# Kernel tuning notes

Measured on AMD Instinct MI355X. Metric: run time of the kernel, lower is better.

## Reference

```python
import jax, jax.numpy as jnp
import numpy as np

B, C, S, E, H = 16, 24, 128, 256, 8
P = E // H  # head projection dim (consistent interpretation of the buggy source)
EPS = 1e-6


def _ln(x, g, b):
    mu = jnp.mean(x, axis=-1, keepdims=True)
    var = jnp.mean((x - mu) ** 2, axis=-1, keepdims=True)
    return (x - mu) * jax.lax.rsqrt(var + EPS) * g + b


def setup_inputs() -> dict:
    key = jax.random.key(0)
    ks = jax.random.split(key, 16)
    s = 0.02
    return {
        'x': jax.random.normal(ks[0], (B, C, S, E), jnp.float32),
        # spatial attention params
        'Wq_s': s * jax.random.normal(ks[1], (H, C, P, E), jnp.float32),
        'Wk_s': s * jax.random.normal(ks[2], (H, E, P), jnp.float32),
        'Wv_s': s * jax.random.normal(ks[3], (H, E, P), jnp.float32),
        'Wo_s': s * jax.random.normal(ks[4], (C, E, E), jnp.float32),
        # temporal attention params
        'Wq_t': s * jax.random.normal(ks[5], (H, C, E, P), jnp.float32),
        'Wk_t': s * jax.random.normal(ks[6], (H, C, E, P), jnp.float32),
        'Wv_t': s * jax.random.normal(ks[7], (H, C, E, P), jnp.float32),
        'Wo_t': s * jax.random.normal(ks[8], (C, E, E), jnp.float32),
        # shared layernorm
        'ln_g': jnp.ones((E,), jnp.float32),
        'ln_b': jnp.zeros((E,), jnp.float32),
        # per-joint pointwise FF (Linear->ReLU->Linear)
        'ff_w1': s * jax.random.normal(ks[9], (C, E, E), jnp.float32),
        'ff_b1': jnp.zeros((C, E), jnp.float32),
        'ff_w2': s * jax.random.normal(ks[10], (C, E, E), jnp.float32),
        'ff_b2': jnp.zeros((C, E), jnp.float32),
    }


def _spatial_attention(x, Wq, Wk, Wv, Wo):
    # x: [B,C,S,E]; per-head per-joint query proj, shared key/value proj
    q = jnp.einsum('bcse,hcpe->bshcp', x, Wq)          # [B,S,H,C,P]
    k = jnp.einsum('bcse,hep->bshcp', x, Wk)
    v = jnp.einsum('bcse,hep->bshcp', x, Wv)
    scores = jnp.einsum('bshcp,bshdp->bshcd', q, k) / jnp.sqrt(jnp.float32(P))
    a = jax.nn.softmax(scores, axis=-1)                # attn over joints d
    o = jnp.einsum('bshcd,bshdp->bshcp', a, v)
    o = o.transpose(0, 3, 1, 2, 4).reshape(x.shape[0], C, x.shape[2], H * P)  # [B,C,S,E]
    return jnp.einsum('bcse,cef->bcsf', o, Wo)


def _temporal_attention(x, Wq, Wk, Wv, Wo):
    q = jnp.einsum('bcse,hcep->bhcsp', x, Wq)          # [B,H,C,S,P]
    k = jnp.einsum('bcse,hcep->bhcsp', x, Wk)
    v = jnp.einsum('bcse,hcep->bhcsp', x, Wv)
    scores = jnp.einsum('bhcsp,bhctp->bhcst', q, k) / jnp.sqrt(jnp.float32(P))
    a = jax.nn.softmax(scores, axis=-1)                # attn over time t
    o = jnp.einsum('bhcst,bhctp->bhcsp', a, v)
    o = o.transpose(0, 2, 3, 1, 4).reshape(x.shape[0], C, x.shape[2], H * P)  # [B,C,S,E]
    return jnp.einsum('bcse,cef->bcsf', o, Wo)


def reference(x, Wq_s, Wk_s, Wv_s, Wo_s, Wq_t, Wk_t, Wv_t, Wo_t, ln_g, ln_b, ff_w1, ff_b1, ff_w2, ff_b2):
    spat = _spatial_attention(x, Wq_s, Wk_s, Wv_s, Wo_s)
    temp = _temporal_attention(x, Wq_t, Wk_t, Wv_t, Wo_t)
    attn_out = _ln(x + spat, ln_g, ln_b) + _ln(x + temp, ln_g, ln_b)
    # per-joint pointwise FF, vectorized over joints
    h = jax.nn.relu(jnp.einsum('bcse,cef->bcsf', attn_out, ff_w1) + ff_b1[None, :, None, :])
    ff = jnp.einsum('bcse,cef->bcsf', h, ff_w2) + ff_b2[None, :, None, :]
    return _ln(attn_out + ff, ln_g, ln_b)
```

## Files before the change

### kernel.cpp

```cpp
#include <hip/hip_runtime.h>
#include <hip/hip_bf16.h>

constexpr int Bn = 16, Cn = 24, Sn = 128, En = 256, Hn = 8, Pn = 32;
constexpr size_t NBUF = (size_t)Bn * Cn * Sn * En;
constexpr size_t WSLOT = (size_t)Cn * 256 * 256;

typedef __bf16 bf16_t;
typedef bf16_t bf16x8 __attribute__((ext_vector_type(8)));
typedef bf16_t bf16x4 __attribute__((ext_vector_type(4)));
typedef float f32x4 __attribute__((ext_vector_type(4)));

__device__ __forceinline__ void gl2lds16(const bf16_t* g, bf16_t* l) {
    typedef const __attribute__((address_space(1))) unsigned int* gp_t;
    typedef __attribute__((address_space(3))) unsigned int* lp_t;
    __builtin_amdgcn_global_load_lds((gp_t)(unsigned long long)g,
                                     (lp_t)(unsigned int)(unsigned long long)l,
                                     16, 0, 0);
}

__global__ __launch_bounds__(256) void conv_x_k(const float* __restrict__ x,
                                                bf16_t* __restrict__ xb) {
    const size_t i = ((size_t)blockIdx.x * 256 + threadIdx.x) * 4;
    const float4 v = *(const float4*)(x + i);
    bf16x4 o = {(bf16_t)v.x, (bf16_t)v.y, (bf16_t)v.z, (bf16_t)v.w};
// ... 1 lines not shown
}

__global__ __launch_bounds__(256) void conv_w_copy_k(const float* __restrict__ W,
                                                     bf16_t* __restrict__ out) {
    const int row = blockIdx.x * 4 + (threadIdx.x >> 6);
    const int lane = threadIdx.x & 63;
    const int n = row & 255, c = row >> 8;
    const float* src = W + (size_t)c * (Pn * En) + (size_t)(n >> 5) * (Cn * Pn * En) +
                       (size_t)(n & 31) * En + lane * 4;
    const float4 v = *(const float4*)src;
    bf16x4 o = {(bf16_t)v.x, (bf16_t)v.y, (bf16_t)v.z, (bf16_t)v.w};
    *(bf16x4*)(out + (size_t)row * 256 + lane * 4) = o;
}

struct TDesc { const float* W; int Sc, Snh, Se; };

__global__ __launch_bounds__(256) void conv_w_tr_k(
    TDesc d0, TDesc d1, TDesc d2, TDesc d3, TDesc d4,
    bf16_t* __restrict__ out)
{
    TDesc d;
    switch (blockIdx.z) {
        case 0: d = d0; break; case 1: d = d1; break; case 2: d = d2; break;
        case 3: d = d3; break; default: d = d4; break;
    }
    const int g = blockIdx.x & 7, et = blockIdx.x >> 3;
    const int c = blockIdx.y;

    __shared__ float tile[32][65];

    const int t = threadIdx.x;
    const float* base = d.W + (size_t)c * d.Sc + (size_t)g * d.Snh;

#pragma unroll
    for (int pass = 0; pass < 2; ++pass) {
        const int e_local = pass * 32 + (t >> 3);
        const int j4 = (t & 7) * 4;
        const float4 v = *(const float4*)(base + (size_t)(et * 64 + e_local) * d.Se + j4);
        tile[j4 + 0][e_local] = v.x;
        tile[j4 + 1][e_local] = v.y;
        tile[j4 + 2][e_local] = v.z;
        tile[j4 + 3][e_local] = v.w;
    }
    __syncthreads();

    const int j = t >> 3, e8 = (t & 7) * 8;
    bf16x8 o;
#pragma unroll
    for (int k = 0; k < 8; ++k) o[k] = (bf16_t)tile[j][e8 + k];
    *(bf16x8*)(out + (size_t)blockIdx.z * WSLOT +
               ((size_t)c * 256 + g * 32 + j) * 256 + et * 64 + e8) = o;
}

__global__ __launch_bounds__(256) void conv_w_k(const float* __restrict__ W,
                                                bf16_t* __restrict__ Wb,
                                                int Sc, int Snh, int Snp, int Se) {
    const int n = blockIdx.x & 255, c = blockIdx.x >> 8;
    const int e = threadIdx.x;
    Wb[(size_t)blockIdx.x * 256 + e] =
        (bf16_t)W[(size_t)c * Sc + (size_t)(n >> 5) * Snh + (n & 31) * Snp + (size_t)e * Se];
}

struct GDesc { const bf16_t* W; bf16_t* O; int Aoff, Wc, Ob, Oc, Os, Onh, Onp, trans; };

template <int NP>
__global__ __launch_bounds__(256) void gemm_mfma(
    const bf16_t* __restrict__ A, int Ab, int Ac, int As,
    GDesc g0, GDesc g1, GDesc g2)
{
    const int b = blockIdx.x, c = blockIdx.z;
    const int proj = (NP == 1) ? 0 : ((int)blockIdx.y >> 1);
    const int nt = (NP == 1) ? (int)blockIdx.y : ((int)blockIdx.y & 1);
    GDesc g = (proj == 0) ? g0 : (proj == 1) ? g1 : g2;

    __shared__ bf16_t smem[3][2][128 * 32];
    bf16_t* Cs = &smem[0][0][0];

    const int tid = threadIdx.x, wv = tid >> 6, ln = tid & 63;
    const int wm = (wv >> 1) * 64, wn = (wv & 1) * 64;
    const int lr = ln & 15, hi = ln >> 4;

    const bf16_t* Abase = A + g.Aoff + (size_t)b * Ab + (size_t)c * Ac;
    const bf16_t* Bbase = g.W + (size_t)c * g.Wc + (size_t)(nt * 128) * 256;

    auto stage = [&](int buf, int kt) {
        const int k0 = kt * 32;
#pragma unroll
        for (int it = 0; it < 2; ++it) {
            const int cb = it * 256 + wv * 64;
            const int mc = cb + ln;
            const int row = mc >> 2;
            const int kc = (((mc & 3) ^ ((row >> 1) & 3)) * 8);
            gl2lds16(Abase + (size_t)row * As + k0 + kc, &smem[buf][0][cb * 8]);
            gl2lds16(Bbase + (size_t)row * 256 + k0 + kc, &smem[buf][1][cb * 8]);
        }
    };

    f32x4 acc[4][4] = {};

    stage(0, 0);
    stage(1, 1);

#pragma unroll
    for (int kt = 0; kt < 8; ++kt) {
        if (kt < 6) stage((kt + 2) % 3, kt + 2);
        if (kt < 6)       asm volatile("s_waitcnt vmcnt(8)" ::: "memory");
        else if (kt == 6) asm volatile("s_waitcnt vmcnt(4)" ::: "memory");
        else              asm volatile("s_waitcnt vmcnt(0)" ::: "memory");
        __builtin_amdgcn_s_barrier();
        __builtin_amdgcn_sched_barrier(0);

        const int cur = kt % 3;
        bf16x8 af[4], bfr[4];
// ... 26 lines not shown
#pragma unroll
                for (int i = 0; i < 4; ++i)
#pragma unroll
                    for (int j = 0; j < 4; ++j)
#pragma unroll
                        for (int r = 0; r < 4; ++r)
                            Cs[(i * 16 + hi * 4 + r) * 136 + wn + j * 16 + lr] =
                                (bf16_t)acc[i][j][r];
            }
            __syncthreads();
#pragma unroll
            for (int it = 0; it < 2; ++it) {
                const int lrow = it * 32 + (tid >> 3);
                const int n0 = (tid & 7) * 16;
                bf16x8 v0 = *(const bf16x8*)&Cs[lrow * 136 + n0];
                bf16x8 v1 = *(const bf16x8*)&Cs[lrow * 136 + n0 + 8];
                const int m = pass * 64 + lrow;
                const int n = nt * 128 + n0;
                bf16_t* dst = g.O + (size_t)b * g.Ob + (size_t)c * g.Oc +
                              (size_t)m * g.Os + (size_t)(n >> 5) * g.Onh + (n & 31);
                *(bf16x8*)dst = v0;
                *(bf16x8*)(dst + 8) = v1;
            }
            __syncthreads();
        } else {
            if (wn == pass * 64) {
#pragma unroll
                for (int i = 0; i < 4; ++i)
#pragma unroll
                    for (int j = 0; j < 4; ++j) {
                        bf16x4 pk = {(bf16_t)acc[i][j][0], (bf16_t)acc[i][j][1],
                                     (bf16_t)acc[i][j][2], (bf16_t)acc[i][j][3]};
                        *(bf16x4*)&Cs[(j * 16 + lr) * 136 + wm + i * 16 + hi * 4] = pk;
                    }
            }
            __syncthreads();
#pragma unroll
            for (int it = 0; it < 2; ++it) {
                const int lrow = it * 32 + (tid >> 3);
                const int m0 = (tid & 7) * 16;
                bf16x8 v0 = *(const bf16x8*)&Cs[lrow * 136 + m0];
                bf16x8 v1 = *(const bf16x8*)&Cs[lrow * 136 + m0 + 8];
                const int n = nt * 128 + pass * 64 + lrow;
                bf16_t* dst = g.O + (size_t)b * g.Ob + (size_t)c * g.Oc +
                              (size_t)(n >> 5) * g.Onh + (size_t)(n & 31) * g.Onp + m0;
                *(bf16x8*)dst = v0;
                *(bf16x8*)(dst + 8) = v1;
            }
            __syncthreads();
        }
    }
}

__global__ __launch_bounds__(256) void wo_ln_fused(
    const bf16_t* __restrict__ A1, const bf16_t* __restrict__ A2,
    const bf16_t* __restrict__ W1, const bf16_t* __restrict__ W2,
    const bf16_t* __restrict__ xb, const float* __restrict__ g,
    const float* __restrict__ beta, bf16_t* __restrict__ AO)
{
    const int bx = blockIdx.x, c = blockIdx.z;
    const int R = ((bx >> 1) * Cn + c) * Sn + (bx & 1) * 64;

    __shared__ bf16_t lds[33792];

    const int tid = threadIdx.x, wv = tid >> 6, ln = tid & 63;
    const int wn = wv * 64, lr = ln & 15, hi = ln >> 4;

    const bf16_t* Ab0 = A1 + (size_t)R * 256;
    const bf16_t* Ab1 = A2 + (size_t)R * 256;
    const bf16_t* Wb0 = W1 + (size_t)c * 65536;
    const bf16_t* Wb1 = W2 + (size_t)c * 65536;

    auto stage = [&](int buf, int t) {
        const bf16_t* Asrc = (t < 8) ? Ab0 : Ab1;
        const bf16_t* Wsrc = (t < 8) ? Wb0 : Wb1;
        const int k0 = (t & 7) * 32;
        bf16_t* base = &lds[buf * 10240];
        {
            const int ch = wv * 64 + ln;
            const int row = ch >> 2;
            const int kc = (((ch & 3) ^ ((row >> 1) & 3)) * 8);
            gl2lds16(Asrc + (size_t)row * 256 + k0 + kc, base + ch * 8);
        }
#pragma unroll
        for (int g2 = 0; g2 < 4; ++g2) {
            const int ch = g2 * 256 + wv * 64 + ln;
            const int row = ch >> 2;
            const int kc = (((ch & 3) ^ ((row >> 1) & 3)) * 8);
            gl2lds16(Wsrc + (size_t)row * 256 + k0 + kc, base + 2048 + ch * 8);
        }
    };

    f32x4 accS[4][4] = {}, accT[4][4] = {};

    stage(0, 0);
#pragma unroll
    for (int t = 0; t < 16; ++t) {
        if (t < 15) {
            stage((t + 1) & 1, t + 1);
            asm volatile("s_waitcnt vmcnt(5)" ::: "memory");
        } else {
            asm volatile("s_waitcnt vmcnt(0)" ::: "memory");
        }
        __builtin_amdgcn_s_barrier();
        __builtin_amdgcn_sched_barrier(0);

        const bf16_t* base = &lds[(t & 1) * 10240];
        bf16x8 af[4], bfr[4];
#pragma unroll
        for (int i = 0; i < 4; ++i) {
            const int r = i * 16 + lr;
            af[i] = *(const bf16x8*)(base + r * 32 + ((hi ^ ((r >> 1) & 3)) * 8));
        }
#pragma unroll
        for (int j = 0; j < 4; ++j) {
            const int r = wn + j * 16 + lr;
            bfr[j] = *(const bf16x8*)(base + 2048 + r * 32 + ((hi ^ ((r >> 1) & 3)) * 8));
        }
        __builtin_amdgcn_s_setprio(1);
        if (t < 8) {
#pragma unroll
            for (int i = 0; i < 4; ++i)
#pragma unroll
                for (int j = 0; j < 4; ++j)
                    accS[i][j] = __builtin_amdgcn_mfma_f32_16x16x32_bf16(af[i], bfr[j], accS[i][j], 0, 0, 0);
        } else {
#pragma unroll
            for (int i = 0; i < 4; ++i)
#pragma unroll
                for (int j = 0; j < 4; ++j)
                    accT[i][j] = __builtin_amdgcn_mfma_f32_16x16x32_bf16(af[i], bfr[j], accT[i][j], 0, 0, 0);
        }
        __builtin_amdgcn_s_setprio(0);
        __builtin_amdgcn_sched_barrier(0);
        __builtin_amdgcn_s_barrier();
    }

    bf16_t* Ss = &lds[0];
    bf16_t* Ts = &lds[16896];
#pragma unroll
    for (int i = 0; i < 4; ++i)
#pragma unroll
        for (int j = 0; j < 4; ++j)
#pragma unroll
            for (int r = 0; r < 4; ++r) {
                const int m = i * 16 + hi * 4 + r;
                const int n = wn + j * 16 + lr;
                Ss[m * 264 + n] = (bf16_t)accS[i][j][r];
                Ts[m * 264 + n] = (bf16_t)accT[i][j][r];
            }
    __syncthreads();

    const int row = tid >> 2, c0 = (tid & 3) * 64;
    const bf16_t* xp = xb + (size_t)(R + row) * 256 + c0;
    bf16x8 xv[8];
    float s1 = 0, q1 = 0, s2 = 0, q2 = 0;
#pragma unroll
    for (int u = 0; u < 8; ++u) {
        xv[u] = *(const bf16x8*)(xp + u * 8);
        bf16x8 sv = *(const bf16x8*)&Ss[row * 264 + c0 + u * 8];
        bf16x8 tv = *(const bf16x8*)&Ts[row * 264 + c0 + u * 8];
#pragma unroll
        for (int e = 0; e < 8; ++e) {
            const float xf = (float)xv[u][e];
            const float a = xf + (float)sv[e];
            const float t2 = xf + (float)tv[e];
            s1 += a; q1 += a * a; s2 += t2; q2 += t2 * t2;
        }
    }
    s1 += __shfl_xor(s1, 1); s1 += __shfl_xor(s1, 2);
    q1 += __shfl_xor(q1, 1); q1 += __shfl_xor(q1, 2);
    s2 += __shfl_xor(s2, 1); s2 += __shfl_xor(s2, 2);
    q2 += __shfl_xor(q2, 1); q2 += __shfl_xor(q2, 2);
    const float mu1 = s1 / 256.f, mu2 = s2 / 256.f;
    const float r1 = rsqrtf(q1 / 256.f - mu1 * mu1 + 1e-6f);
    const float r2 = rsqrtf(q2 / 256.f - mu2 * mu2 + 1e-6f);
#pragma unroll
    for (int u = 0; u < 8; ++u) {
        bf16x8 sv = *(const bf16x8*)&Ss[row * 264 + c0 + u * 8];
        bf16x8 tv = *(const bf16x8*)&Ts[row * 264 + c0 + u * 8];
        bf16x8 o8;
#pragma unroll
        for (int e = 0; e < 8; ++e) {
            const int n = c0 + u * 8 + e;
            const float xf = (float)xv[u][e];
            const float a = xf + (float)sv[e];
            const float t2 = xf + (float)tv[e];
            o8[e] = (bf16_t)((a - mu1) * r1 * g[n] + (t2 - mu2) * r2 * g[n] + 2.f * beta[n]);
        }
        *(bf16x8*)(AO + (size_t)(R + row) * 256 + c0 + u * 8) = o8;
    }
}

__global__ __launch_bounds__(256) void ff_ln_fused(
    const bf16_t* __restrict__ AO, const bf16_t* __restrict__ W1,
    const bf16_t* __restrict__ W2, const float* __restrict__ b1v,
    const float* __restrict__ b2v, const float* __restrict__ g,
    const float* __restrict__ beta, float* __restrict__ out)
{
    const int bx = blockIdx.x, c = blockIdx.z;
    const int R = ((bx >> 1) * Cn + c) * Sn + (bx & 1) * 64;

    __shared__ bf16_t lds[37376];

    const int tid = threadIdx.x, wv = tid >> 6, ln = tid & 63;
    const int wn = wv * 64, lr = ln & 15, hi = ln >> 4;

    const bf16_t* Abase = AO + (size_t)R * 256;
    const bf16_t* W1b = W1 + (size_t)c * 65536;
    const bf16_t* W2b = W2 + (size_t)c * 65536;
    bf16_t* Hs = &lds[20480];

    auto stageA = [&](int buf, int kt) {
        const int k0 = kt * 32;
        const int ch = wv * 64 + ln;
        const int row = ch >> 2;
        const int kc = (((ch & 3) ^ ((row >> 1) & 3)) * 8);
        gl2lds16(Abase + (size_t)row * 256 + k0 + kc, &lds[buf * 10240] + ch * 8);
    };
    auto stageB = [&](int buf, int kt, const bf16_t* Wsrc) {
        const int k0 = kt * 32;
#pragma unroll
        for (int g2 = 0; g2 < 4; ++g2) {
            const int ch = g2 * 256 + wv * 64 + ln;
            const int row = ch >> 2;
            const int kc = (((ch & 3) ^ ((row >> 1) & 3)) * 8);
            gl2lds16(Wsrc + (size_t)row * 256 + k0 + kc, &lds[buf * 10240] + 2048 + ch * 8);
        }
    };

    f32x4 acc[4][4] = {};

    stageA(0, 0); stageB(0, 0, W1b);
#pragma unroll
    for (int t = 0; t < 8; ++t) {
        if (t < 7) {
            stageA((t + 1) & 1, t + 1); stageB((t + 1) & 1, t + 1, W1b);
            asm volatile("s_waitcnt vmcnt(5)" ::: "memory");
        } else {
            asm volatile("s_waitcnt vmcnt(0)" ::: "memory");
        }
        __builtin_amdgcn_s_barrier();
        __builtin_amdgcn_sched_barrier(0);
        const bf16_t* base = &lds[(t & 1) * 10240];
        bf16x8 af[4], bfr[4];
#pragma unroll
        for (int i = 0; i < 4; ++i) {
            const int r = i * 16 + lr;
            af[i] = *(const bf16x8*)(base + r * 32 + ((hi ^ ((r >> 1) & 3)) * 8));
        }
#pragma unroll
        for (int j = 0; j < 4; ++j) {
            const int r = wn + j * 16 + lr;
            bfr[j] = *(const bf16x8*)(base + 2048 + r * 32 + ((hi ^ ((r >> 1) & 3)) * 8));
        }
        __builtin_amdgcn_s_setprio(1);
#pragma unroll
        for (int i = 0; i < 4; ++i)
#pragma unroll
            for (int j = 0; j < 4; ++j)
                acc[i][j] = __builtin_amdgcn_mfma_f32_16x16x32_bf16(af[i], bfr[j], acc[i][j], 0, 0, 0);
        __builtin_amdgcn_s_setprio(0);
        __builtin_amdgcn_sched_barrier(0);
        __builtin_amdgcn_s_barrier();
    }

    stageB(0, 0, W2b);
#pragma unroll
    for (int i = 0; i < 4; ++i)
#pragma unroll
        for (int j = 0; j < 4; ++j) {
            const int n = wn + j * 16 + lr;
            const float bv = b1v[c * 256 + n];
#pragma unroll
            for (int r = 0; r < 4; ++r)
                Hs[(i * 16 + hi * 4 + r) * 264 + n] =
                    (bf16_t)fmaxf(acc[i][j][r] + bv, 0.f);
        }
    __syncthreads();

    f32x4 acc2[4][4] = {};
#pragma unroll
    for (int t = 0; t < 8; ++t) {
        if (t < 7) {
            stageB((t + 1) & 1, t + 1, W2b);
            asm volatile("s_waitcnt vmcnt(4)" ::: "memory");
        } else {
            asm volatile("s_waitcnt vmcnt(0)" ::: "memory");
        }
        __builtin_amdgcn_s_barrier();
        __builtin_amdgcn_sched_barrier(0);
        const bf16_t* base = &lds[(t & 1) * 10240];
        bf16x8 af[4], bfr[4];
#pragma unroll
        for (int i = 0; i < 4; ++i)
            af[i] = *(const bf16x8*)&Hs[(i * 16 + lr) * 264 + t * 32 + hi * 8];
#pragma unroll
        for (int j = 0; j < 4; ++j) {
            const int r = wn + j * 16 + lr;
            bfr[j] = *(const bf16x8*)(base + 2048 + r * 32 + ((hi ^ ((r >> 1) & 3)) * 8));
        }
        __builtin_amdgcn_s_setprio(1);
#pragma unroll
        for (int i = 0; i < 4; ++i)
#pragma unroll
            for (int j = 0; j < 4; ++j)
                acc2[i][j] = __builtin_amdgcn_mfma_f32_16x16x32_bf16(af[i], bfr[j], acc2[i][j], 0, 0, 0);
        __builtin_amdgcn_s_setprio(0);
        __builtin_amdgcn_sched_barrier(0);
        __builtin_amdgcn_s_barrier();
    }

    bf16_t* Fs = &lds[0];
#pragma unroll
    for (int i = 0; i < 4; ++i)
#pragma unroll
        for (int j = 0; j < 4; ++j) {
            const int n = wn + j * 16 + lr;
            const float bv = b2v[c * 256 + n];
#pragma unroll
            for (int r = 0; r < 4; ++r)
                Fs[(i * 16 + hi * 4 + r) * 264 + n] = (bf16_t)(acc2[i][j][r] + bv);
        }
    __syncthreads();

    const int row = tid >> 2, c0 = (tid & 3) * 64;
    const bf16_t* ap = AO + (size_t)(R + row) * 256 + c0;
    bf16x8 av[8];
    float s = 0, q = 0;
#pragma unroll
    for (int u = 0; u < 8; ++u) {
        av[u] = *(const bf16x8*)(ap + u * 8);
        bf16x8 fv = *(const bf16x8*)&Fs[row * 264 + c0 + u * 8];
#pragma unroll
        for (int e = 0; e < 8; ++e) {
            const float a = (float)av[u][e] + (float)fv[e];
            s += a; q += a * a;
        }
    }
    s += __shfl_xor(s, 1); s += __shfl_xor(s, 2);
    q += __shfl_xor(q, 1); q += __shfl_xor(q, 2);
    const float mu = s / 256.f;
    const float rin = rsqrtf(q / 256.f - mu * mu + 1e-6f);
#pragma unroll
    for (int u = 0; u < 8; ++u) {
        bf16x8 fv = *(const bf16x8*)&Fs[row * 264 + c0 + u * 8];
        float4 o0, o1;
        float* op = &o0.x;
#pragma unroll
        for (int e = 0; e < 8; ++e) {
            const int n = c0 + u * 8 + e;
            const float a = (float)av[u][e] + (float)fv[e];
            const float v = (a - mu) * rin * g[n] + beta[n];
            if (e < 4) (&o0.x)[e] = v; else (&o1.x)[e - 4] = v;
        }
        (void)op;
        float* dst = out + (size_t)(R + row) * 256 + c0 + u * 8;
        *(float4*)dst = o0;
        *(float4*)(dst + 4) = o1;
    }
}

__global__ __launch_bounds__(256) void attn_spatial_mfma(
    const bf16_t* __restrict__ Q, const bf16_t* __restrict__ K,
    const bf16_t* __restrict__ V, bf16_t* __restrict__ O)
{
    __shared__ bf16_t Ps[4][32 * 40];
    __shared__ bf16_t Vt[4][32 * 40];

    const int tid = threadIdx.x, wv = tid >> 6, ln = tid & 63;
    const int lr = ln & 15, hi = ln >> 4, lk = hi * 8;

    const int bsh = blockIdx.x * 4 + wv;
    const int h = bsh & 7, s = (bsh >> 3) & 127, b = bsh >> 10;
    const size_t qb = (size_t)bsh * (Cn * Pn);

    {
        const int p = ln >> 1, c0 = 24 + (ln & 1) * 4;
        bf16x4 z = {};
        *(bf16x4*)&Vt[wv][p * 40 + c0] = z;
    }
#pragma unroll
    for (int it = 0; it < 2; ++it) {
        const int ch = it * 64 + ln;
        if (ch < 96) {
            const int cc = ch >> 2, p0 = (ch & 3) * 8;
            bf16x8 v = *(const bf16x8*)(V + qb + cc * 32 + p0);
#pragma unroll
            for (int j = 0; j < 8; ++j)
                Vt[wv][(p0 + j) * 40 + cc] = v[j];
        }
    }

    bf16x8 aq0 = *(const bf16x8*)(Q + qb + lr * 32 + lk);
    bf16x8 aq1 = *(const bf16x8*)(Q + qb + (16 + lr) * 32 + lk);
    bf16x8 bk0 = *(const bf16x8*)(K + qb + lr * 32 + lk);
    bf16x8 bk1 = *(const bf16x8*)(K + qb + (16 + lr) * 32 + lk);
    const f32x4 zz = {0.f, 0.f, 0.f, 0.f};
    f32x4 sc[2][2];
    sc[0][0] = __builtin_amdgcn_mfma_f32_16x16x32_bf16(aq0, bk0, zz, 0, 0, 0);
    sc[0][1] = __builtin_amdgcn_mfma_f32_16x16x32_bf16(aq0, bk1, zz, 0, 0, 0);
    sc[1][0] = __builtin_amdgcn_mfma_f32_16x16x32_bf16(aq1, bk0, zz, 0, 0, 0);
    sc[1][1] = __builtin_amdgcn_mfma_f32_16x16x32_bf16(aq1, bk1, zz, 0, 0, 0);

    const float scale = 0.17677669529663687f;
#pragma unroll
    for (int i = 0; i < 2; ++i) {
        float s0[4], s1[4], mx[4];
#pragma unroll
        for (int r = 0; r < 4; ++r) {
            s0[r] = sc[i][0][r] * scale;
            s1[r] = (lr >= 8) ? -3.0e38f : sc[i][1][r] * scale;
// ... 139 lines not shown
        bf16x8 bv0 = *(const bf16x8*)&Vs[lr * 136 + kk * 32 + lk];
        bf16x8 bv1 = *(const bf16x8*)&Vs[(16 + lr) * 136 + kk * 32 + lk];
        o[0][0] = __builtin_amdgcn_mfma_f32_16x16x32_bf16(ap0, bv0, o[0][0], 0, 0, 0);
        o[0][1] = __builtin_amdgcn_mfma_f32_16x16x32_bf16(ap0, bv1, o[0][1], 0, 0, 0);
        o[1][0] = __builtin_amdgcn_mfma_f32_16x16x32_bf16(ap1, bv0, o[1][0], 0, 0, 0);
        o[1][1] = __builtin_amdgcn_mfma_f32_16x16x32_bf16(ap1, bv1, o[1][1], 0, 0, 0);
    }

#pragma unroll
    for (int i = 0; i < 2; ++i) {
        const int sb = r0 + i * 16 + (ln >> 4) * 4;
#pragma unroll
        for (int j = 0; j < 2; ++j) {
            const int p = h * 32 + j * 16 + lr;
#pragma unroll
            for (int r = 0; r < 4; ++r)
                O[((size_t)(b * Cn + c) * Sn + (sb + r)) * En + p] = (bf16_t)o[i][j][r];
        }
    }
}

extern "C" void kernel_launch(void* const* d_in, const int* in_sizes, int n_in,
                              void* d_out, int out_size, void* d_ws, size_t ws_size,
                              hipStream_t stream)
{
    const float* x     = (const float*)d_in[0];
    const float* Wq_s  = (const float*)d_in[1];
    const float* Wk_s  = (const float*)d_in[2];
    const float* Wv_s  = (const float*)d_in[3];
    const float* Wo_s  = (const float*)d_in[4];
    const float* Wq_t  = (const float*)d_in[5];
    const float* Wk_t  = (const float*)d_in[6];
    const float* Wv_t  = (const float*)d_in[7];
    const float* Wo_t  = (const float*)d_in[8];
    const float* ln_g  = (const float*)d_in[9];
    const float* ln_b  = (const float*)d_in[10];
    const float* ff_w1 = (const float*)d_in[11];
    const float* ff_b1 = (const float*)d_in[12];
    const float* ff_w2 = (const float*)d_in[13];
    const float* ff_b2 = (const float*)d_in[14];
    float* out = (float*)d_out;

    bf16_t* wsb = (bf16_t*)d_ws;
    bf16_t* b0 = wsb;
    bf16_t* b1 = wsb + NBUF;
    bf16_t* b2 = wsb + 2 * NBUF;
    bf16_t* b3 = wsb + 3 * NBUF;
    bf16_t* b4 = wsb + 4 * NBUF;

    bf16_t* xb = (bf16_t*)d_out;
    bf16_t* wb = xb + NBUF;
    bf16_t* w_qs = wb + 0 * WSLOT;
    bf16_t* wtr  = wb + 1 * WSLOT;
    bf16_t* w_os = wtr + 0 * WSLOT;
    bf16_t* w_qt = wtr + 1 * WSLOT;
    bf16_t* w_kt = wtr + 2 * WSLOT;
    bf16_t* w_vt = wtr + 3 * WSLOT;
    bf16_t* w_ot = wtr + 4 * WSLOT;
    bf16_t* w_ks = b4 + NBUF - 2 * 65536;
    bf16_t* w_vs = b4 + NBUF - 65536;
    bf16_t* w_f1 = b0;
    bf16_t* w_f2 = b0 + WSLOT;

    const int XAb = Cn * Sn * En, XAc = Sn * En, XAs = En;
    const int QSb = Sn * Hn * Cn * Pn, QSs = Hn * Cn * Pn, QSh = Cn * Pn;
    const int QTb = Hn * Cn * Sn * Pn, QTh = Cn * Sn * Pn, QTc = Sn * Pn, QTs = Pn;
    const int WCP = 256 * 256;

    conv_x_k<<<NBUF / 1024, 256, 0, stream>>>(x, xb);
    conv_w_copy_k<<<1536, 256, 0, stream>>>(Wq_s, w_qs);
    conv_w_tr_k<<<dim3(32, 24, 5), 256, 0, stream>>>(
        TDesc{Wo_s, En * En, Pn, En},
        TDesc{Wq_t, En * Pn, Cn * En * Pn, Pn},
        TDesc{Wk_t, En * Pn, Cn * En * Pn, Pn},
        TDesc{Wv_t, En * Pn, Cn * En * Pn, Pn},
        TDesc{Wo_t, En * En, Pn, En},
        wtr);
    conv_w_k<<<256, 256, 0, stream>>>(Wk_s, w_ks, 0, En * Pn, 1, Pn);
    conv_w_k<<<256, 256, 0, stream>>>(Wv_s, w_vs, 0, En * Pn, 1, Pn);

    gemm_mfma<3><<<dim3(16, 6, 24), 256, 0, stream>>>(
        xb, XAb, XAc, XAs,
        GDesc{w_qs, b0, 0, WCP, QSb, Pn, QSs, QSh, 1, 0},
        GDesc{w_ks, b1, 0, 0,   QSb, Pn, QSs, QSh, 1, 0},
        GDesc{w_vs, b2, 0, 0,   QSb, Pn, QSs, QSh, 1, 0});
    attn_spatial_mfma<<<Bn * Sn * Hn / 4, 256, 0, stream>>>(b0, b1, b2, b3);

    gemm_mfma<3><<<dim3(16, 6, 24), 256, 0, stream>>>(
        xb, XAb, XAc, XAs,
        GDesc{w_qt, b0, 0, WCP, QTb, QTc, QTs, QTh, 1, 0},
        GDesc{w_kt, b1, 0, WCP, QTb, QTc, QTs, QTh, 1, 0},
        GDesc{w_vt, b2, 0, WCP, QTb, QTc, 1, QTh, Sn, 1});
    attn_temporal_mfma<<<dim3(24, 8, 16), 256, 0, stream>>>(b0, b1, b2, b4);

    conv_w_tr_k<<<dim3(32, 24, 2), 256, 0, stream>>>(
        TDesc{ff_w1, En * En, Pn, En},
        TDesc{ff_w2, En * En, Pn, En},
        TDesc{ff_w1, En * En, Pn, En},
        TDesc{ff_w1, En * En, Pn, En},
        TDesc{ff_w1, En * En, Pn, En},
        w_f1);

    wo_ln_fused<<<dim3(32, 1, 24), 256, 0, stream>>>(
        b3, b4, w_os, w_ot, xb, ln_g, ln_b, b2);

    ff_ln_fused<<<dim3(32, 1, 24), 256, 0, stream>>>(
        b2, w_f1, w_f2, ff_b1, ff_b2, ln_g, ln_b, out);
}
```

Measured before the change: 387.3 us.

## Fuse output projections, layernorms and feed-forward into one epilogue kernel

Merges the Wo/LayerNorm kernel and the FF/LayerNorm kernel into a single epilogue kernel. The attention-sum activation now stays in registers and LDS instead of going to global memory as bf16 and being read back. The two Wo GEMMs run in sequence with a shared accumulator to lower register pressure. The residual x is read directly as fp32 rather than from the bf16 copy. Weight conversion launches are also regrouped: the Wk_s/Wv_s conversions become one launch, and the Wo transposes move to the later conversion launch. In exchange the kernel is longer and has more barriers.

```diff
diff --git a/kernel.cpp b/kernel.cpp
--- a/kernel.cpp
+++ b/kernel.cpp
@@ -77,13 +77,15 @@
                ((size_t)c * 256 + g * 32 + j) * 256 + et * 64 + e8) = o;
 }
 
-__global__ __launch_bounds__(256) void conv_w_k(const float* __restrict__ W,
-                                                bf16_t* __restrict__ Wb,
-                                                int Sc, int Snh, int Snp, int Se) {
-    const int n = blockIdx.x & 255, c = blockIdx.x >> 8;
-    const int e = threadIdx.x;
-    Wb[(size_t)blockIdx.x * 256 + e] =
-        (bf16_t)W[(size_t)c * Sc + (size_t)(n >> 5) * Snh + (n & 31) * Snp + (size_t)e * Se];
+__global__ __launch_bounds__(256) void conv_w_k2(const float* __restrict__ Wk,
+                                                 const float* __restrict__ Wv,
+                                                 bf16_t* __restrict__ Ok,
+                                                 bf16_t* __restrict__ Ov) {
+    const float* W = blockIdx.y ? Wv : Wk;
+    bf16_t* o = blockIdx.y ? Ov : Ok;
+    const int n = blockIdx.x, e = threadIdx.x;
+    o[(size_t)n * 256 + e] =
+        (bf16_t)W[(size_t)(n >> 5) * (En * Pn) + (n & 31) + (size_t)e * Pn];
 }
 
 struct GDesc { const bf16_t* W; bf16_t* O; int Aoff, Wc, Ob, Oc, Os, Onh, Onp, trans; };
@@ -216,149 +218,11 @@
     }
 }
 
-__global__ __launch_bounds__(256) void wo_ln_fused(
+__global__ __launch_bounds__(256) void epilogue_fused(
     const bf16_t* __restrict__ A1, const bf16_t* __restrict__ A2,
-    const bf16_t* __restrict__ W1, const bf16_t* __restrict__ W2,
-    const bf16_t* __restrict__ xb, const float* __restrict__ g,
-    const float* __restrict__ beta, bf16_t* __restrict__ AO)
-{
-    const int bx = blockIdx.x, c = blockIdx.z;
-    const int R = ((bx >> 1) * Cn + c) * Sn + (bx & 1) * 64;
-
-    __shared__ bf16_t lds[33792];
-
-    const int tid = threadIdx.x, wv = tid >> 6, ln = tid & 63;
-    const int wn = wv * 64, lr = ln & 15, hi = ln >> 4;
-
-    const bf16_t* Ab0 = A1 + (size_t)R * 256;
-    const bf16_t* Ab1 = A2 + (size_t)R * 256;
-    const bf16_t* Wb0 = W1 + (size_t)c * 65536;
-    const bf16_t* Wb1 = W2 + (size_t)c * 65536;
-
-    auto stage = [&](int buf, int t) {
-        const bf16_t* Asrc = (t < 8) ? Ab0 : Ab1;
-        const bf16_t* Wsrc = (t < 8) ? Wb0 : Wb1;
-        const int k0 = (t & 7) * 32;
-        bf16_t* base = &lds[buf * 10240];
-        {
-            const int ch = wv * 64 + ln;
-            const int row = ch >> 2;
-            const int kc = (((ch & 3) ^ ((row >> 1) & 3)) * 8);
-            gl2lds16(Asrc + (size_t)row * 256 + k0 + kc, base + ch * 8);
-        }
-#pragma unroll
-        for (int g2 = 0; g2 < 4; ++g2) {
-            const int ch = g2 * 256 + wv * 64 + ln;
-            const int row = ch >> 2;
-            const int kc = (((ch & 3) ^ ((row >> 1) & 3)) * 8);
-            gl2lds16(Wsrc + (size_t)row * 256 + k0 + kc, base + 2048 + ch * 8);
-        }
-    };
-
-    f32x4 accS[4][4] = {}, accT[4][4] = {};
-
-    stage(0, 0);
-#pragma unroll
-    for (int t = 0; t < 16; ++t) {
-        if (t < 15) {
-            stage((t + 1) & 1, t + 1);
-            asm volatile("s_waitcnt vmcnt(5)" ::: "memory");
-        } else {
-            asm volatile("s_waitcnt vmcnt(0)" ::: "memory");
-        }
-        __builtin_amdgcn_s_barrier();
-        __builtin_amdgcn_sched_barrier(0);
-
-        const bf16_t* base = &lds[(t & 1) * 10240];
-        bf16x8 af[4], bfr[4];
-#pragma unroll
-        for (int i = 0; i < 4; ++i) {
-            const int r = i * 16 + lr;
-            af[i] = *(const bf16x8*)(base + r * 32 + ((hi ^ ((r >> 1) & 3)) * 8));
-        }
-#pragma unroll
-        for (int j = 0; j < 4; ++j) {
-            const int r = wn + j * 16 + lr;
-            bfr[j] = *(const bf16x8*)(base + 2048 + r * 32 + ((hi ^ ((r >> 1) & 3)) * 8));
-        }
-        __builtin_amdgcn_s_setprio(1);
-        if (t < 8) {
-#pragma unroll
-            for (int i = 0; i < 4; ++i)
-#pragma unroll
-                for (int j = 0; j < 4; ++j)
-                    accS[i][j] = __builtin_amdgcn_mfma_f32_16x16x32_bf16(af[i], bfr[j], accS[i][j], 0, 0, 0);
-        } else {
-#pragma unroll
-            for (int i = 0; i < 4; ++i)
-#pragma unroll
-                for (int j = 0; j < 4; ++j)
-                    accT[i][j] = __builtin_amdgcn_mfma_f32_16x16x32_bf16(af[i], bfr[j], accT[i][j], 0, 0, 0);
-        }
-        __builtin_amdgcn_s_setprio(0);
-        __builtin_amdgcn_sched_barrier(0);
-        __builtin_amdgcn_s_barrier();
-    }
-
-    bf16_t* Ss = &lds[0];
-    bf16_t* Ts = &lds[16896];
-#pragma unroll
-    for (int i = 0; i < 4; ++i)
-#pragma unroll
-        for (int j = 0; j < 4; ++j)
-#pragma unroll
-            for (int r = 0; r < 4; ++r) {
-                const int m = i * 16 + hi * 4 + r;
-                const int n = wn + j * 16 + lr;
-                Ss[m * 264 + n] = (bf16_t)accS[i][j][r];
-                Ts[m * 264 + n] = (bf16_t)accT[i][j][r];
-            }
-    __syncthreads();
-
-    const int row = tid >> 2, c0 = (tid & 3) * 64;
-    const bf16_t* xp = xb + (size_t)(R + row) * 256 + c0;
-    bf16x8 xv[8];
-    float s1 = 0, q1 = 0, s2 = 0, q2 = 0;
-#pragma unroll
-    for (int u = 0; u < 8; ++u) {
-        xv[u] = *(const bf16x8*)(xp + u * 8);
-        bf16x8 sv = *(const bf16x8*)&Ss[row * 264 + c0 + u * 8];
-        bf16x8 tv = *(const bf16x8*)&Ts[row * 264 + c0 + u * 8];
-#pragma unroll
-        for (int e = 0; e < 8; ++e) {
-            const float xf = (float)xv[u][e];
-            const float a = xf + (float)sv[e];
-            const float t2 = xf + (float)tv[e];
-            s1 += a; q1 += a * a; s2 += t2; q2 += t2 * t2;
-        }
-    }
-    s1 += __shfl_xor(s1, 1); s1 += __shfl_xor(s1, 2);
-    q1 += __shfl_xor(q1, 1); q1 += __shfl_xor(q1, 2);
-    s2 += __shfl_xor(s2, 1); s2 += __shfl_xor(s2, 2);
-    q2 += __shfl_xor(q2, 1); q2 += __shfl_xor(q2, 2);
-    const float mu1 = s1 / 256.f, mu2 = s2 / 256.f;
-    const float r1 = rsqrtf(q1 / 256.f - mu1 * mu1 + 1e-6f);
-    const float r2 = rsqrtf(q2 / 256.f - mu2 * mu2 + 1e-6f);
-#pragma unroll
-    for (int u = 0; u < 8; ++u) {
-        bf16x8 sv = *(const bf16x8*)&Ss[row * 264 + c0 + u * 8];
-        bf16x8 tv = *(const bf16x8*)&Ts[row * 264 + c0 + u * 8];
-        bf16x8 o8;
-#pragma unroll
-        for (int e = 0; e < 8; ++e) {
-            const int n = c0 + u * 8 + e;
-            const float xf = (float)xv[u][e];
-            const float a = xf + (float)sv[e];
-            const float t2 = xf + (float)tv[e];
-            o8[e] = (bf16_t)((a - mu1) * r1 * g[n] + (t2 - mu2) * r2 * g[n] + 2.f * beta[n]);
-        }
-        *(bf16x8*)(AO + (size_t)(R + row) * 256 + c0 + u * 8) = o8;
-    }
-}
-
-__global__ __launch_bounds__(256) void ff_ln_fused(
-    const bf16_t* __restrict__ AO, const bf16_t* __restrict__ W1,
-    const bf16_t* __restrict__ W2, const float* __restrict__ b1v,
+    const bf16_t* __restrict__ Wos, const bf16_t* __restrict__ Wot,
+    const bf16_t* __restrict__ Wf1, const bf16_t* __restrict__ Wf2,
+    const float* __restrict__ xf, const float* __restrict__ b1v,
     const float* __restrict__ b2v, const float* __restrict__ g,
     const float* __restrict__ beta, float* __restrict__ out)
 {
@@ -369,67 +233,244 @@
 
     const int tid = threadIdx.x, wv = tid >> 6, ln = tid & 63;
     const int wn = wv * 64, lr = ln & 15, hi = ln >> 4;
-
-    const bf16_t* Abase = AO + (size_t)R * 256;
-    const bf16_t* W1b = W1 + (size_t)c * 65536;
-    const bf16_t* W2b = W2 + (size_t)c * 65536;
-    bf16_t* Hs = &lds[20480];
-
-    auto stageA = [&](int buf, int kt) {
+    const int row = tid >> 2, c0 = (tid & 3) * 64;
+
+    const bf16_t* WosB = Wos + (size_t)c * 65536;
+    const bf16_t* WotB = Wot + (size_t)c * 65536;
+    const bf16_t* W1b  = Wf1 + (size_t)c * 65536;
+    const bf16_t* W2b  = Wf2 + (size_t)c * 65536;
+
+    auto stageAW = [&](int buf, int kt, const bf16_t* Asrc, const bf16_t* Wsrc) {
         const int k0 = kt * 32;
-        const int ch = wv * 64 + ln;
-        const int row = ch >> 2;
-        const int kc = (((ch & 3) ^ ((row >> 1) & 3)) * 8);
-        gl2lds16(Abase + (size_t)row * 256 + k0 + kc, &lds[buf * 10240] + ch * 8);
-    };
-    auto stageB = [&](int buf, int kt, const bf16_t* Wsrc) {
-        const int k0 = kt * 32;
+        bf16_t* base = &lds[buf * 10240];
+        {
+            const int ch = wv * 64 + ln;
+            const int r2 = ch >> 2;
+            const int kc = (((ch & 3) ^ ((r2 >> 1) & 3)) * 8);
+            gl2lds16(Asrc + (size_t)r2 * 256 + k0 + kc, base + ch * 8);
+        }
 #pragma unroll
         for (int g2 = 0; g2 < 4; ++g2) {
             const int ch = g2 * 256 + wv * 64 + ln;
-            const int row = ch >> 2;
-            const int kc = (((ch & 3) ^ ((row >> 1) & 3)) * 8);
-            gl2lds16(Wsrc + (size_t)row * 256 + k0 + kc, &lds[buf * 10240] + 2048 + ch * 8);
+            const int r2 = ch >> 2;
+            const int kc = (((ch & 3) ^ ((r2 >> 1) & 3)) * 8);
+            gl2lds16(Wsrc + (size_t)r2 * 256 + k0 + kc, base + 2048 + ch * 8);
         }
     };
-
-    f32x4 acc[4][4] = {};
-
-    stageA(0, 0); stageB(0, 0, W1b);
-#pragma unroll
-    for (int t = 0; t < 8; ++t) {
-        if (t < 7) {
-            stageA((t + 1) & 1, t + 1); stageB((t + 1) & 1, t + 1, W1b);
-            asm volatile("s_waitcnt vmcnt(5)" ::: "memory");
-        } else {
-            asm volatile("s_waitcnt vmcnt(0)" ::: "memory");
-        }
-        __builtin_amdgcn_s_barrier();
-        __builtin_amdgcn_sched_barrier(0);
-        const bf16_t* base = &lds[(t & 1) * 10240];
-        bf16x8 af[4], bfr[4];
-#pragma unroll
-        for (int i = 0; i < 4; ++i) {
-            const int r = i * 16 + lr;
-            af[i] = *(const bf16x8*)(base + r * 32 + ((hi ^ ((r >> 1) & 3)) * 8));
-        }
-#pragma unroll
-        for (int j = 0; j < 4; ++j) {
-            const int r = wn + j * 16 + lr;
-            bfr[j] = *(const bf16x8*)(base + 2048 + r * 32 + ((hi ^ ((r >> 1) & 3)) * 8));
-        }
-        __builtin_amdgcn_s_setprio(1);
+    auto stageW = [&](int buf, int kt, const bf16_t* Wsrc) {
+        const int k0 = kt * 32;
+#pragma unroll
+        for (int g2 = 0; g2 < 4; ++g2) {
+            const int ch = g2 * 256 + wv * 64 + ln;
+            const int r2 = ch >> 2;
+            const int kc = (((ch & 3) ^ ((r2 >> 1) & 3)) * 8);
+            gl2lds16(Wsrc + (size_t)r2 * 256 + k0 + kc,
+                     &lds[20480 + buf * 8192] + ch * 8);
+        }
+    };
+
+    f32x4 acc[4][4];
+    bf16x8 ao_r[8], xv_r[8];
+    bf16_t* STs = &lds[20480];
+
+    {
+        const bf16_t* Ab = A1 + (size_t)R * 256;
 #pragma unroll
         for (int i = 0; i < 4; ++i)
 #pragma unroll
-            for (int j = 0; j < 4; ++j)
-                acc[i][j] = __builtin_amdgcn_mfma_f32_16x16x32_bf16(af[i], bfr[j], acc[i][j], 0, 0, 0);
-        __builtin_amdgcn_s_setprio(0);
-        __builtin_amdgcn_sched_barrier(0);
-        __builtin_amdgcn_s_barrier();
-    }
-
-    stageB(0, 0, W2b);
+            for (int j = 0; j < 4; ++j) acc[i][j] = (f32x4){0.f, 0.f, 0.f, 0.f};
+        stageAW(0, 0, Ab, WosB);
+#pragma unroll
+        for (int t = 0; t < 8; ++t) {
+            if (t < 7) {
+                stageAW((t + 1) & 1, t + 1, Ab, WosB);
+                asm volatile("s_waitcnt vmcnt(5)" ::: "memory");
+            } else asm volatile("s_waitcnt vmcnt(0)" ::: "memory");
+            __builtin_amdgcn_s_barrier();
+            __builtin_amdgcn_sched_barrier(0);
+            const bf16_t* base = &lds[(t & 1) * 10240];
+            bf16x8 af[4], bfr[4];
+#pragma unroll
+            for (int i = 0; i < 4; ++i) {
+                const int r = i * 16 + lr;
+                af[i] = *(const bf16x8*)(base + r * 32 + ((hi ^ ((r >> 1) & 3)) * 8));
+            }
+#pragma unroll
+            for (int j = 0; j < 4; ++j) {
+                const int r = wn + j * 16 + lr;
+                bfr[j] = *(const bf16x8*)(base + 2048 + r * 32 + ((hi ^ ((r >> 1) & 3)) * 8));
+            }
+            __builtin_amdgcn_s_setprio(1);
+#pragma unroll
+            for (int i = 0; i < 4; ++i)
+#pragma unroll
+                for (int j = 0; j < 4; ++j)
+                    acc[i][j] = __builtin_amdgcn_mfma_f32_16x16x32_bf16(af[i], bfr[j], acc[i][j], 0, 0, 0);
+            __builtin_amdgcn_s_setprio(0);
+            __builtin_amdgcn_sched_barrier(0);
+            __builtin_amdgcn_s_barrier();
+        }
+    }
+#pragma unroll
+    for (int i = 0; i < 4; ++i)
+#pragma unroll
+        for (int j = 0; j < 4; ++j)
+#pragma unroll
+            for (int r = 0; r < 4; ++r)
+                STs[(i * 16 + hi * 4 + r) * 264 + wn + j * 16 + lr] = (bf16_t)acc[i][j][r];
+    __syncthreads();
+
+    const bf16_t* Ab2 = A2 + (size_t)R * 256;
+    stageAW(0, 0, Ab2, WotB);
+
+    {
+        const float* xp = xf + (size_t)(R + row) * 256 + c0;
+        float s1 = 0, q1 = 0;
+#pragma unroll
+        for (int u = 0; u < 8; ++u) {
+            const float4 xa = *(const float4*)(xp + u * 8);
+            const float4 xb4 = *(const float4*)(xp + u * 8 + 4);
+            bf16x8 xv;
+            xv[0] = (bf16_t)xa.x; xv[1] = (bf16_t)xa.y; xv[2] = (bf16_t)xa.z; xv[3] = (bf16_t)xa.w;
+            xv[4] = (bf16_t)xb4.x; xv[5] = (bf16_t)xb4.y; xv[6] = (bf16_t)xb4.z; xv[7] = (bf16_t)xb4.w;
+            xv_r[u] = xv;
+            bf16x8 sv = *(const bf16x8*)&STs[row * 264 + c0 + u * 8];
+#pragma unroll
+            for (int e = 0; e < 8; ++e) {
+                const float a = (float)xv[e] + (float)sv[e];
+                s1 += a; q1 += a * a;
+            }
+        }
+        s1 += __shfl_xor(s1, 1); s1 += __shfl_xor(s1, 2);
+        q1 += __shfl_xor(q1, 1); q1 += __shfl_xor(q1, 2);
+        const float mu1 = s1 / 256.f;
+        const float r1 = rsqrtf(q1 / 256.f - mu1 * mu1 + 1e-6f);
+#pragma unroll
+        for (int u = 0; u < 8; ++u) {
+            bf16x8 sv = *(const bf16x8*)&STs[row * 264 + c0 + u * 8];
+            bf16x8 o8;
+#pragma unroll
+            for (int e = 0; e < 8; ++e) {
+                const int n = c0 + u * 8 + e;
+                const float a = (float)xv_r[u][e] + (float)sv[e];
+                o8[e] = (bf16_t)((a - mu1) * r1 * g[n] + beta[n]);
+            }
+            ao_r[u] = o8;
+        }
+    }
+
+    {
+#pragma unroll
+        for (int i = 0; i < 4; ++i)
+#pragma unroll
+            for (int j = 0; j < 4; ++j) acc[i][j] = (f32x4){0.f, 0.f, 0.f, 0.f};
+#pragma unroll
+        for (int t = 0; t < 8; ++t) {
+            if (t < 7) {
+                stageAW((t + 1) & 1, t + 1, Ab2, WotB);
+                asm volatile("s_waitcnt vmcnt(5)" ::: "memory");
+            } else asm volatile("s_waitcnt vmcnt(0)" ::: "memory");
+            __builtin_amdgcn_s_barrier();
+            __builtin_amdgcn_sched_barrier(0);
+            const bf16_t* base = &lds[(t & 1) * 10240];
+            bf16x8 af[4], bfr[4];
+#pragma unroll
+            for (int i = 0; i < 4; ++i) {
+                const int r = i * 16 + lr;
+                af[i] = *(const bf16x8*)(base + r * 32 + ((hi ^ ((r >> 1) & 3)) * 8));
+            }
+#pragma unroll
+            for (int j = 0; j < 4; ++j) {
+                const int r = wn + j * 16 + lr;
+                bfr[j] = *(const bf16x8*)(base + 2048 + r * 32 + ((hi ^ ((r >> 1) & 3)) * 8));
+            }
+            __builtin_amdgcn_s_setprio(1);
+#pragma unroll
+            for (int i = 0; i < 4; ++i)
+#pragma unroll
+                for (int j = 0; j < 4; ++j)
+                    acc[i][j] = __builtin_amdgcn_mfma_f32_16x16x32_bf16(af[i], bfr[j], acc[i][j], 0, 0, 0);
+            __builtin_amdgcn_s_setprio(0);
+            __builtin_amdgcn_sched_barrier(0);
+            __builtin_amdgcn_s_barrier();
+        }
+    }
+#pragma unroll
+    for (int i = 0; i < 4; ++i)
+#pragma unroll
+        for (int j = 0; j < 4; ++j)
+#pragma unroll
+            for (int r = 0; r < 4; ++r)
+                STs[(i * 16 + hi * 4 + r) * 264 + wn + j * 16 + lr] = (bf16_t)acc[i][j][r];
+    __syncthreads();
+
+    {
+        float s2 = 0, q2 = 0;
+#pragma unroll
+        for (int u = 0; u < 8; ++u) {
+            bf16x8 tv = *(const bf16x8*)&STs[row * 264 + c0 + u * 8];
+#pragma unroll
+            for (int e = 0; e < 8; ++e) {
+                const float a = (float)xv_r[u][e] + (float)tv[e];
+                s2 += a; q2 += a * a;
+            }
+        }
+        s2 += __shfl_xor(s2, 1); s2 += __shfl_xor(s2, 2);
+        q2 += __shfl_xor(q2, 1); q2 += __shfl_xor(q2, 2);
+        const float mu2 = s2 / 256.f;
+        const float r2 = rsqrtf(q2 / 256.f - mu2 * mu2 + 1e-6f);
+#pragma unroll
+        for (int u = 0; u < 8; ++u) {
+            bf16x8 tv = *(const bf16x8*)&STs[row * 264 + c0 + u * 8];
+            bf16x8 o8;
+#pragma unroll
+            for (int e = 0; e < 8; ++e) {
+                const int n = c0 + u * 8 + e;
+                const float a = (float)xv_r[u][e] + (float)tv[e];
+                o8[e] = (bf16_t)((float)ao_r[u][e] + (a - mu2) * r2 * g[n] + beta[n]);
+            }
+            ao_r[u] = o8;
+            *(bf16x8*)&lds[row * 264 + c0 + u * 8] = o8;
+        }
+    }
+    __syncthreads();
+
+    {
+#pragma unroll
+        for (int i = 0; i < 4; ++i)
+#pragma unroll
+            for (int j = 0; j < 4; ++j) acc[i][j] = (f32x4){0.f, 0.f, 0.f, 0.f};
+        stageW(0, 0, W1b);
+#pragma unroll
+        for (int t = 0; t < 8; ++t) {
+            if (t < 7) {
+                stageW((t + 1) & 1, t + 1, W1b);
+                asm volatile("s_waitcnt vmcnt(4)" ::: "memory");
+            } else asm volatile("s_waitcnt vmcnt(0)" ::: "memory");
+            __builtin_amdgcn_s_barrier();
+            __builtin_amdgcn_sched_barrier(0);
+            bf16x8 af[4], bfr[4];
+#pragma unroll
+            for (int i = 0; i < 4; ++i)
+                af[i] = *(const bf16x8*)&lds[(i * 16 + lr) * 264 + t * 32 + hi * 8];
+#pragma unroll
+            for (int j = 0; j < 4; ++j) {
+                const int r = wn + j * 16 + lr;
+                bfr[j] = *(const bf16x8*)(&lds[20480 + (t & 1) * 8192] + r * 32 +
+                                          ((hi ^ ((r >> 1) & 3)) * 8));
+            }
+            __builtin_amdgcn_s_setprio(1);
+#pragma unroll
+            for (int i = 0; i < 4; ++i)
+#pragma unroll
+                for (int j = 0; j < 4; ++j)
+                    acc[i][j] = __builtin_amdgcn_mfma_f32_16x16x32_bf16(af[i], bfr[j], acc[i][j], 0, 0, 0);
+            __builtin_amdgcn_s_setprio(0);
+            __builtin_amdgcn_sched_barrier(0);
+            __builtin_amdgcn_s_barrier();
+        }
+    }
+    stageW(0, 0, W2b);
 #pragma unroll
     for (int i = 0; i < 4; ++i)
 #pragma unroll
@@ -438,44 +479,45 @@
             const float bv = b1v[c * 256 + n];
 #pragma unroll
             for (int r = 0; r < 4; ++r)
-                Hs[(i * 16 + hi * 4 + r) * 264 + n] =
+                lds[(i * 16 + hi * 4 + r) * 264 + n] =
                     (bf16_t)fmaxf(acc[i][j][r] + bv, 0.f);
         }
     __syncthreads();
 
-    f32x4 acc2[4][4] = {};
-#pragma unroll
-    for (int t = 0; t < 8; ++t) {
-        if (t < 7) {
-            stageB((t + 1) & 1, t + 1, W2b);
-            asm volatile("s_waitcnt vmcnt(4)" ::: "memory");
-        } else {
-            asm volatile("s_waitcnt vmcnt(0)" ::: "memory");
-        }
-        __builtin_amdgcn_s_barrier();
-        __builtin_amdgcn_sched_barrier(0);
-        const bf16_t* base = &lds[(t & 1) * 10240];
-        bf16x8 af[4], bfr[4];
+    {
 #pragma unroll
         for (int i = 0; i < 4; ++i)
-            af[i] = *(const bf16x8*)&Hs[(i * 16 + lr) * 264 + t * 32 + hi * 8];
-#pragma unroll
-        for (int j = 0; j < 4; ++j) {
-            const int r = wn + j * 16 + lr;
-            bfr[j] = *(const bf16x8*)(base + 2048 + r * 32 + ((hi ^ ((r >> 1) & 3)) * 8));
-        }
-        __builtin_amdgcn_s_setprio(1);
-#pragma unroll
-        for (int i = 0; i < 4; ++i)
-#pragma unroll
-            for (int j = 0; j < 4; ++j)
-                acc2[i][j] = __builtin_amdgcn_mfma_f32_16x16x32_bf16(af[i], bfr[j], acc2[i][j], 0, 0, 0);
-        __builtin_amdgcn_s_setprio(0);
-        __builtin_amdgcn_sched_barrier(0);
-        __builtin_amdgcn_s_barrier();
-    }
-
-    bf16_t* Fs = &lds[0];
+#pragma unroll
+            for (int j = 0; j < 4; ++j) acc[i][j] = (f32x4){0.f, 0.f, 0.f, 0.f};
+#pragma unroll
+        for (int t = 0; t < 8; ++t) {
+            if (t < 7) {
+                stageW((t + 1) & 1, t + 1, W2b);
+                asm volatile("s_waitcnt vmcnt(4)" ::: "memory");
+            } else asm volatile("s_waitcnt vmcnt(0)" ::: "memory");
+            __builtin_amdgcn_s_barrier();
+            __builtin_amdgcn_sched_barrier(0);
+            bf16x8 af[4], bfr[4];
+#pragma unroll
+            for (int i = 0; i < 4; ++i)
+                af[i] = *(const bf16x8*)&lds[(i * 16 + lr) * 264 + t * 32 + hi * 8];
+#pragma unroll
+            for (int j = 0; j < 4; ++j) {
+                const int r = wn + j * 16 + lr;
+                bfr[j] = *(const bf16x8*)(&lds[20480 + (t & 1) * 8192] + r * 32 +
+                                          ((hi ^ ((r >> 1) & 3)) * 8));
+            }
+            __builtin_amdgcn_s_setprio(1);
+#pragma unroll
+            for (int i = 0; i < 4; ++i)
+#pragma unroll
+                for (int j = 0; j < 4; ++j)
+                    acc[i][j] = __builtin_amdgcn_mfma_f32_16x16x32_bf16(af[i], bfr[j], acc[i][j], 0, 0, 0);
+            __builtin_amdgcn_s_setprio(0);
+            __builtin_amdgcn_sched_barrier(0);
+            __builtin_amdgcn_s_barrier();
+        }
+    }
 #pragma unroll
     for (int i = 0; i < 4; ++i)
 #pragma unroll
@@ -484,44 +526,40 @@
             const float bv = b2v[c * 256 + n];
 #pragma unroll
             for (int r = 0; r < 4; ++r)
-                Fs[(i * 16 + hi * 4 + r) * 264 + n] = (bf16_t)(acc2[i][j][r] + bv);
+                STs[(i * 16 + hi * 4 + r) * 264 + n] = (bf16_t)(acc[i][j][r] + bv);
         }
     __syncthreads();
 
-    const int row = tid >> 2, c0 = (tid & 3) * 64;
-    const bf16_t* ap = AO + (size_t)(R + row) * 256 + c0;
-    bf16x8 av[8];
-    float s = 0, q = 0;
-#pragma unroll
-    for (int u = 0; u < 8; ++u) {
-        av[u] = *(const bf16x8*)(ap + u * 8);
-        bf16x8 fv = *(const bf16x8*)&Fs[row * 264 + c0 + u * 8];
-#pragma unroll
-        for (int e = 0; e < 8; ++e) {
-            const float a = (float)av[u][e] + (float)fv[e];
-            s += a; q += a * a;
-        }
-    }
-    s += __shfl_xor(s, 1); s += __shfl_xor(s, 2);
-    q += __shfl_xor(q, 1); q += __shfl_xor(q, 2);
-    const float mu = s / 256.f;
-    const float rin = rsqrtf(q / 256.f - mu * mu + 1e-6f);
-#pragma unroll
-    for (int u = 0; u < 8; ++u) {
-        bf16x8 fv = *(const bf16x8*)&Fs[row * 264 + c0 + u * 8];
-        float4 o0, o1;
-        float* op = &o0.x;
-#pragma unroll
-        for (int e = 0; e < 8; ++e) {
-            const int n = c0 + u * 8 + e;
-            const float a = (float)av[u][e] + (float)fv[e];
-            const float v = (a - mu) * rin * g[n] + beta[n];
-            if (e < 4) (&o0.x)[e] = v; else (&o1.x)[e - 4] = v;
-        }
-        (void)op;
-        float* dst = out + (size_t)(R + row) * 256 + c0 + u * 8;
-        *(float4*)dst = o0;
-        *(float4*)(dst + 4) = o1;
+    {
+        float s = 0, q = 0;
+#pragma unroll
+        for (int u = 0; u < 8; ++u) {
+            bf16x8 fv = *(const bf16x8*)&STs[row * 264 + c0 + u * 8];
+#pragma unroll
+            for (int e = 0; e < 8; ++e) {
+                const float a = (float)ao_r[u][e] + (float)fv[e];
+                s += a; q += a * a;
+            }
+        }
+        s += __shfl_xor(s, 1); s += __shfl_xor(s, 2);
+        q += __shfl_xor(q, 1); q += __shfl_xor(q, 2);
+        const float mu = s / 256.f;
+        const float rin = rsqrtf(q / 256.f - mu * mu + 1e-6f);
+#pragma unroll
+        for (int u = 0; u < 8; ++u) {
+            bf16x8 fv = *(const bf16x8*)&STs[row * 264 + c0 + u * 8];
+            float4 o0, o1;
+#pragma unroll
+            for (int e = 0; e < 8; ++e) {
+                const int n = c0 + u * 8 + e;
+                const float a = (float)ao_r[u][e] + (float)fv[e];
+                const float v = (a - mu) * rin * g[n] + beta[n];
+                if (e < 4) (&o0.x)[e] = v; else (&o1.x)[e - 4] = v;
+            }
+            float* dst = out + (size_t)(R + row) * 256 + c0 + u * 8;
+            *(float4*)dst = o0;
+            *(float4*)(dst + 4) = o1;
+        }
     }
 }
 
@@ -767,15 +805,15 @@
     bf16_t* wb = xb + NBUF;
     bf16_t* w_qs = wb + 0 * WSLOT;
     bf16_t* wtr  = wb + 1 * WSLOT;
-    bf16_t* w_os = wtr + 0 * WSLOT;
-    bf16_t* w_qt = wtr + 1 * WSLOT;
-    bf16_t* w_kt = wtr + 2 * WSLOT;
-    bf16_t* w_vt = wtr + 3 * WSLOT;
-    bf16_t* w_ot = wtr + 4 * WSLOT;
+    bf16_t* w_qt = wtr + 0 * WSLOT;
+    bf16_t* w_kt = wtr + 1 * WSLOT;
+    bf16_t* w_vt = wtr + 2 * WSLOT;
     bf16_t* w_ks = b4 + NBUF - 2 * 65536;
     bf16_t* w_vs = b4 + NBUF - 65536;
-    bf16_t* w_f1 = b0;
-    bf16_t* w_f2 = b0 + WSLOT;
+    bf16_t* w_os = b0;
+    bf16_t* w_ot = b0 + WSLOT;
+    bf16_t* w_f1 = b0 + 2 * WSLOT;
+    bf16_t* w_f2 = b0 + 3 * WSLOT;
 
     const int XAb = Cn * Sn * En, XAc = Sn * En, XAs = En;
     const int QSb = Sn * Hn * Cn * Pn, QSs = Hn * Cn * Pn, QSh = Cn * Pn;
@@ -784,15 +822,14 @@
 
     conv_x_k<<<NBUF / 1024, 256, 0, stream>>>(x, xb);
     conv_w_copy_k<<<1536, 256, 0, stream>>>(Wq_s, w_qs);
-    conv_w_tr_k<<<dim3(32, 24, 5), 256, 0, stream>>>(
-        TDesc{Wo_s, En * En, Pn, En},
+    conv_w_tr_k<<<dim3(32, 24, 3), 256, 0, stream>>>(
         TDesc{Wq_t, En * Pn, Cn * En * Pn, Pn},
         TDesc{Wk_t, En * Pn, Cn * En * Pn, Pn},
         TDesc{Wv_t, En * Pn, Cn * En * Pn, Pn},
-        TDesc{Wo_t, En * En, Pn, En},
+        TDesc{Wq_t, En * Pn, Cn * En * Pn, Pn},
+        TDesc{Wq_t, En * Pn, Cn * En * Pn, Pn},
         wtr);
-    conv_w_k<<<256, 256, 0, stream>>>(Wk_s, w_ks, 0, En * Pn, 1, Pn);
-    conv_w_k<<<256, 256, 0, stream>>>(Wv_s, w_vs, 0, En * Pn, 1, Pn);
+    conv_w_k2<<<dim3(256, 2), 256, 0, stream>>>(Wk_s, Wv_s, w_ks, w_vs);
 
     gemm_mfma<3><<<dim3(16, 6, 24), 256, 0, stream>>>(
         xb, XAb, XAc, XAs,
@@ -808,17 +845,14 @@
         GDesc{w_vt, b2, 0, WCP, QTb, QTc, 1, QTh, Sn, 1});
     attn_temporal_mfma<<<dim3(24, 8, 16), 256, 0, stream>>>(b0, b1, b2, b4);
 
-    conv_w_tr_k<<<dim3(32, 24, 2), 256, 0, stream>>>(
+    conv_w_tr_k<<<dim3(32, 24, 4), 256, 0, stream>>>(
+        TDesc{Wo_s, En * En, Pn, En},
+        TDesc{Wo_t, En * En, Pn, En},
         TDesc{ff_w1, En * En, Pn, En},
         TDesc{ff_w2, En * En, Pn, En},
-        TDesc{ff_w1, En * En, Pn, En},
-        TDesc{ff_w1, En * En, Pn, En},
-        TDesc{ff_w1, En * En, Pn, En},
-        w_f1);
-
-    wo_ln_fused<<<dim3(32, 1, 24), 256, 0, stream>>>(
-        b3, b4, w_os, w_ot, xb, ln_g, ln_b, b2);
-
-    ff_ln_fused<<<dim3(32, 1, 24), 256, 0, stream>>>(
-        b2, w_f1, w_f2, ff_b1, ff_b2, ln_g, ln_b, out);
-}
+        TDesc{Wo_s, En * En, Pn, En},
+        b0);
+
+    epilogue_fused<<<dim3(32, 1, 24), 256, 0, stream>>>(
+        b3, b4, w_os, w_ot, w_f1, w_f2, x, ff_b1, ff_b2, ln_g, ln_b, out);
+}
```

Measured after the change: 393.7 us. No clear change (+1.6%).
